# Kernel tuning notes

Measured on AMD Instinct MI355X. Metric: run time of the kernel, lower is better.

## Reference

```python
import jax, jax.numpy as jnp
from jax import lax
import numpy as np

B, C, L = 32, 8, 512
C_IN = 512      # must equal L (tokenConv consumes permuted tensor)
D_MODEL = 512
SCALE_NUM = 64  # 63 actual scales


def build_wavelet_bank(scale_num, LB=-8.0, UB=8.0, N=1024, Fb=2.0, Fc=8.0):
    """Replicates cmor_torch; returns centered zero-padded kernel bank [S, K].
    Zero-centering is exact because every kernel length (16*s+1) is odd and K is odd,
    so the padded conv with pad=(K-1)//2 equals the original per-scale conv with
    pad=(k-1)//2."""
    x = np.linspace(LB, UB, N)
    wav = (np.pi * Fb) ** (-0.5) * np.exp(2j * np.pi * Fc * x) * np.exp(-x ** 2 / Fb)
    step = x[1] - x[0]
    kernels = []
    for scale in np.arange(1, scale_num):
        j = (np.arange(scale * (x[-1] - x[0]) + 1) / (scale * step)).astype(int)
        j = j[j < wav.size]
        kernels.append(np.real(wav[j]) * scale ** (-0.5))
    K = max(len(k) for k in kernels)
    if K % 2 == 0:
        K += 1
    bank = np.zeros((len(kernels), K), np.float32)
    for i, k in enumerate(kernels):
        assert (K - len(k)) % 2 == 0, "kernel parity mismatch"
        off = (K - len(k)) // 2
        bank[i, off:off + len(k)] = k
    return bank


def setup_inputs() -> dict:
    key = jax.random.key(0)
    k1, k2 = jax.random.split(key)
    x = jax.random.normal(k1, (B, C, L), dtype=jnp.float32)
    wavelet_bank = jnp.asarray(build_wavelet_bank(SCALE_NUM))  # [63, K]
    token_w = jax.random.normal(k2, (D_MODEL, C_IN, 3), dtype=jnp.float32) * 0.02
    return {"x": x, "wavelet_bank": wavelet_bank, "token_w": token_w}


def reference(x, wavelet_bank, token_w):
    Bb, Cc, Ll = x.shape
    S, K = wavelet_bank.shape
    pad = (K - 1) // 2
    # fused CWT over all (channel, scale) pairs: [B*C, 1, L] conv [S, 1, K] -> [B*C, S, L]
    xr = x.reshape(Bb * Cc, 1, Ll)
    conv = lax.conv_general_dilated(
        xr, wavelet_bank[:, None, :], window_strides=(1,),
        padding=[(pad, pad)], dimension_numbers=("NCH", "OIH", "NCH"))
    d = jnp.abs(jnp.diff(conv, axis=-1))                 # [B*C, S, L-1]
    d = jnp.concatenate([d, d[..., -1:]], axis=-1)       # replicate last sample -> L
    feats = d.reshape(Bb, Cc * S, Ll)
    out = jnp.concatenate([x, feats], axis=1)            # [B, C*(1+S), L]
    # tokenConv on permuted tensor: channels = L (= c_in), length = C*(1+S)
    h = out.transpose(0, 2, 1)                           # [B, L, C_total]
    hp = jnp.concatenate([h[..., -1:], h, h[..., :1]], axis=-1)  # circular pad=1
    y = lax.conv_general_dilated(
        hp, token_w, window_strides=(1,), padding="VALID",
        dimension_numbers=("NCH", "OIH", "NCH"))         # [B, d_model, C_total]
    return y.transpose(0, 2, 1)                          # [B, C_total, d_model]
```

## Files before the change

kernel.cpp:

```cpp
#include <hip/hip_runtime.h>
#include <hip/hip_bf16.h>

#define NB 32
#define NC 8
#define NL 512
#define NS 63
#define NK 1009
#define NPAD 504
#define ND 512
#define NCT 512
#define NROWS 514

typedef __attribute__((ext_vector_type(4))) float f32x4;
typedef __attribute__((ext_vector_type(8))) short short8;
typedef __attribute__((ext_vector_type(4))) short short4v;

#define APAD_BYTES (NB * NROWS * NL * 2)
#define WB_BYTES   (3 * ND * NL * 2)
#define BANKB_BYTES (64 * 1024 * 2)

typedef const __attribute__((address_space(1))) unsigned int* gp1_t;
typedef __attribute__((address_space(3))) unsigned int* lp3_t;
__device__ __forceinline__ void gload_lds16(const void* g, void* l) {
  __builtin_amdgcn_global_load_lds((gp1_t)g, (lp3_t)l, 16, 0, 0);
}

__device__ __forceinline__ unsigned short bf16_bits(float v) {
  return __builtin_bit_cast(unsigned short, __float2bfloat16(v));
}

#define WAITVM(N) asm volatile("s_waitcnt vmcnt(" #N ")" ::: "memory")
#define FENCE() asm volatile("" ::: "memory")
#define BAR() __builtin_amdgcn_s_barrier()

__global__ __launch_bounds__(256) void prep_kernel(
    const float* __restrict__ bank, const float* __restrict__ tw,
    __hip_bfloat16* __restrict__ Wb, __hip_bfloat16* __restrict__ bankB) {
  const int idx = blockIdx.x * 256 + threadIdx.x;
  const int stride = gridDim.x * 256;

  for (int i = idx; i < ND * NL; i += stride) {
    float w0 = tw[i * 3 + 0];
    float w1 = tw[i * 3 + 1];
    float w2 = tw[i * 3 + 2];
    Wb[0 * ND * NL + i] = __float2bfloat16(w0);
    Wb[1 * ND * NL + i] = __float2bfloat16(w1);
    Wb[2 * ND * NL + i] = __float2bfloat16(w2);
  }
  for (int i = idx; i < 64 * 1024; i += stride) {
    int s = i >> 10;
    int k = i & 1023;
    float v = (s < NS && k < NK) ? bank[s * NK + k] : 0.f;
    bankB[i] = __float2bfloat16(v);
  }
}

#define CPY_STRIDE 3088

__global__ __launch_bounds__(512) void cwt_kernel(
    const float* __restrict__ x, const __hip_bfloat16* __restrict__ bankB,
    __hip_bfloat16* __restrict__ Apad) {
  __shared__ char smem[32768 + 4 * CPY_STRIDE];
  char* bankS = smem;
  char* cpy = smem + 32768;

  const int tid = threadIdx.x;
  const int bc = blockIdx.x;
  const int b = bc >> 3, c = bc & 7;
  const int w = tid >> 6, l = tid & 63;
  const int hi = l >> 4, li = l & 15;

  const float* xrow = x + bc * NL;

  {
    __hip_bfloat16 v = __float2bfloat16(xrow[tid & 511]);
    if (tid < 512) {
      Apad[((size_t)(b * NROWS) + 1 + c) * NL + tid] = v;
      if (c == 0) Apad[((size_t)(b * NROWS) + 513) * NL + tid] = v;
    }
  }

  for (int i = 0; i < 6; ++i) {
    int p = tid + i * 512;
    int r = p / 768, pe = p - r * 768;
    int e0 = 2 * pe;
    int i0 = e0 + r;
    float xa = (i0 >= NPAD && i0 < NPAD + NL) ? xrow[i0 - NPAD] : 0.f;
    float xb = (i0 + 1 >= NPAD && i0 + 1 < NPAD + NL) ? xrow[i0 + 1 - NPAD] : 0.f;
    float xc = (i0 + 2 >= NPAD && i0 + 2 < NPAD + NL) ? xrow[i0 + 2 - NPAD] : 0.f;
    unsigned short u0 = bf16_bits(xb - xa);
    unsigned short u1 = bf16_bits(xc - xb);
    *(unsigned int*)(cpy + r * CPY_STRIDE + e0 * 2) = (unsigned)u0 | ((unsigned)u1 << 16);
  }

#define STAGE(kt, buf)                                                        \
  {                                                                           \
    for (int i = 0; i < 2; ++i) {                                             \
      int ck = tid + i * 512;                                                 \
      int s_ = ck >> 4, rb = ck & 15;                                         \
      int srcc = rb ^ (s_ & 7);                                               \
      gload_lds16(bankB + s_ * 1024 + (kt) * 128 + srcc * 8,                  \
                  bankS + (buf) * 16384 + ck * 16);                           \
    }                                                                         \
  }

  STAGE(0, 0);
  __syncthreads();

  f32x4 acc[4][4] = {};
  const int r = l & 3;
  const int tbase = w * 64;
  int buf = 0;

  for (int kt = 0; kt < 8; ++kt) {
    if (kt < 7) STAGE(kt + 1, buf ^ 1);

#pragma unroll
    for (int ksl = 0; ksl < 4; ++ksl) {
      short8 av[4], bv[4];
#pragma unroll
      for (int m = 0; m < 4; ++m) {
        int srow = m * 16 + li;
        int chunk = (ksl * 4 + hi) ^ (srow & 7);
        av[m] = *(const short8*)(bankS + buf * 16384 + srow * 256 + chunk * 16);
      }
#pragma unroll
      for (int n = 0; n < 4; ++n) {
        int t = tbase + n * 16 + li;
        int e = t - r + kt * 128 + ksl * 32 + hi * 8;
        const char* pc = cpy + r * CPY_STRIDE + e * 2;
        short4v lo = *(const short4v*)pc;
        short4v hh = *(const short4v*)(pc + 8);
        short8 f;
        f[0] = lo[0]; f[1] = lo[1]; f[2] = lo[2]; f[3] = lo[3];
        f[4] = hh[0]; f[5] = hh[1]; f[6] = hh[2]; f[7] = hh[3];
        bv[n] = f;
      }
#pragma unroll
      for (int m = 0; m < 4; ++m)
#pragma unroll
        for (int n = 0; n < 4; ++n)
          acc[m][n] = __builtin_amdgcn_mfma_f32_16x16x32_bf16(av[m], bv[n], acc[m][n], 0, 0, 0);
    }

    if (kt < 7) {
      __syncthreads();
      buf ^= 1;
    }
  }

#pragma unroll
  for (int m = 0; m < 4; ++m) {
#pragma unroll
    for (int rg = 0; rg < 4; ++rg) {
      int s = m * 16 + hi * 4 + rg;
      if (s >= NS) continue;
      int ch = 8 + c * NS + s;
      size_t rowbase = ((size_t)(b * NROWS) + 1 + ch) * NL;
#pragma unroll
      for (int n = 0; n < 4; ++n) {
        int t = tbase + n * 16 + li;
        float d = fabsf(acc[m][n][rg]);
        __hip_bfloat16 hv = __float2bfloat16(d);
        bool lastgrp = (w == 7 && n == 3);
        bool skip = lastgrp && (li == 15);
        bool dup = lastgrp && (li == 14);
        if (!skip) Apad[rowbase + t] = hv;
        if (dup) Apad[rowbase + 511] = hv;
        if (ch == NCT - 1) {
          size_t wrapbase = (size_t)(b * NROWS) * NL;
          if (!skip) Apad[wrapbase + t] = hv;
          if (dup) Apad[wrapbase + 511] = hv;
        }
      }
    }
  }
#undef STAGE
}

__global__ __launch_bounds__(256) void gemm_kernel(
    const __hip_bfloat16* __restrict__ Ap, const __hip_bfloat16* __restrict__ Wb,
    float* __restrict__ out) {
  __shared__ __hip_bfloat16 sA[3][128 * 32];
  __shared__ __hip_bfloat16 sB[3][128 * 32];

  const int tid = threadIdx.x;
  const int b = blockIdx.y;
  const int tile = blockIdx.x;
  const int p0 = (tile & 3) * 128;
  const int o0 = (tile >> 2) * 128;

  const int w = tid >> 6, lane = tid & 63;
  const int wm = w >> 1, wn = w & 1;
  const int row_in = lane & 15, hi = lane >> 4;

  const int r0 = tid >> 2, cg0 = (tid & 3) ^ ((r0 >> 1) & 3);
  const int ck1 = tid + 256;
  const int r1 = ck1 >> 2, cg1 = (ck1 & 3) ^ ((r1 >> 1) & 3);

#define GSTAGE(kk, bu)                                                         \
  {                                                                            \
    const int kap_ = (kk) >> 4;                                                \
    const int l0_ = ((kk) & 15) << 5;                                          \
    gload_lds16(Ap + ((b * NROWS + p0 + kap_ + r0) * NL + l0_ + cg0 * 8),      \
                &sA[bu][tid * 8]);                                             \
    gload_lds16(Ap + ((b * NROWS + p0 + kap_ + r1) * NL + l0_ + cg1 * 8),      \
                &sA[bu][ck1 * 8]);                                             \
    gload_lds16(Wb + ((kap_ * ND + o0 + r0) * NL + l0_ + cg0 * 8),             \
                &sB[bu][tid * 8]);                                             \
    gload_lds16(Wb + ((kap_ * ND + o0 + r1) * NL + l0_ + cg1 * 8),             \
                &sB[bu][ck1 * 8]);                                             \
  }

#define COMPUTE(bu)                                                            \
  {                                                                            \
    short8 av[4], bv[4];                                                       \
    _Pragma("unroll") for (int m = 0; m < 4; ++m) {                            \
      int row = wm * 64 + m * 16 + row_in;                                     \
      int slot = row * 4 + (hi ^ ((row >> 1) & 3));                            \
      av[m] = *(const short8*)(&sA[bu][slot * 8]);                             \
    }                                                                          \
    _Pragma("unroll") for (int n = 0; n < 4; ++n) {                            \
      int row = wn * 64 + n * 16 + row_in;                                     \
      int slot = row * 4 + (hi ^ ((row >> 1) & 3));                            \
      bv[n] = *(const short8*)(&sB[bu][slot * 8]);                             \
    }                                                                          \
    _Pragma("unroll") for (int m = 0; m < 4; ++m)                              \
      _Pragma("unroll") for (int n = 0; n < 4; ++n)                            \
        acc[m][n] = __builtin_amdgcn_mfma_f32_16x16x32_bf16(av[m], bv[n],      \
                                                            acc[m][n], 0, 0, 0); \
  }

  f32x4 acc[4][4] = {};

  GSTAGE(0, 0);
  GSTAGE(1, 1);

  for (int g = 0; g < 15; ++g) {
    const int kk = g * 3;
    GSTAGE(kk + 2, 2); WAITVM(8); BAR(); FENCE(); COMPUTE(0); FENCE(); BAR();
    GSTAGE(kk + 3, 0); WAITVM(8); BAR(); FENCE(); COMPUTE(1); FENCE(); BAR();
    GSTAGE(kk + 4, 1); WAITVM(8); BAR(); FENCE(); COMPUTE(2); FENCE(); BAR();
  }
  GSTAGE(47, 2); WAITVM(8); BAR(); FENCE(); COMPUTE(0); FENCE(); BAR();
  WAITVM(4); BAR(); FENCE(); COMPUTE(1); FENCE(); BAR();
  WAITVM(0); BAR(); FENCE(); COMPUTE(2);
#undef GSTAGE
#undef COMPUTE

#pragma unroll
  for (int m = 0; m < 4; ++m) {
    const int p = p0 + wm * 64 + m * 16 + hi * 4;
#pragma unroll
    for (int n = 0; n < 4; ++n) {
      const int o = o0 + wn * 64 + n * 16 + row_in;
#pragma unroll
      for (int r = 0; r < 4; ++r)
        out[(size_t)((b * NCT) + p + r) * ND + o] = acc[m][n][r];
    }
  }
}

extern "C" void kernel_launch(void* const* d_in, const int* in_sizes, int n_in,
                              void* d_out, int out_size, void* d_ws, size_t ws_size,
                              hipStream_t stream) {
  const float* x = (const float*)d_in[0];
  const float* bank = (const float*)d_in[1];
  const float* tw = (const float*)d_in[2];
  float* out = (float*)d_out;

  char* ws = (char*)d_ws;
  __hip_bfloat16* Apad = (__hip_bfloat16*)ws;
  __hip_bfloat16* Wb = (__hip_bfloat16*)(ws + APAD_BYTES);
  __hip_bfloat16* bankB = (__hip_bfloat16*)(ws + APAD_BYTES + WB_BYTES);

  prep_kernel<<<512, 256, 0, stream>>>(bank, tw, Wb, bankB);
  cwt_kernel<<<256, 512, 0, stream>>>(x, bankB, Apad);
  gemm_kernel<<<dim3(16, 32), 256, 0, stream>>>(Apad, Wb, out);
}
```

Baseline: 68.57 us.

## Vectorize prep, preload whole CWT bank, 4-stage GEMM pipeline with block swizzle

The prep kernel now has each thread convert four weight triplets at once with float4 loads and ushort4 stores, and the launch shrinks to 256 blocks. The CWT kernel loads all eight bank K-tiles into 128KB of LDS up front and waits on them step by step with vmcnt, replacing the double-buffer loop and its syncs. The GEMM kernel moves to a 4-deep LDS ring with one barrier per stage and remaps block IDs so neighbouring blocks share batch tiles for better L2 reuse. The larger LDS footprints may reduce occupancy, and removing the trailing barrier relies on the 4-buffer distance to stay race-free.

```diff
diff --git a/kernel.cpp b/kernel.cpp
--- a/kernel.cpp
+++ b/kernel.cpp
@@ -37,21 +37,22 @@
     const float* __restrict__ bank, const float* __restrict__ tw,
     __hip_bfloat16* __restrict__ Wb, __hip_bfloat16* __restrict__ bankB) {
   const int idx = blockIdx.x * 256 + threadIdx.x;
-  const int stride = gridDim.x * 256;
-
-  for (int i = idx; i < ND * NL; i += stride) {
-    float w0 = tw[i * 3 + 0];
-    float w1 = tw[i * 3 + 1];
-    float w2 = tw[i * 3 + 2];
-    Wb[0 * ND * NL + i] = __float2bfloat16(w0);
-    Wb[1 * ND * NL + i] = __float2bfloat16(w1);
-    Wb[2 * ND * NL + i] = __float2bfloat16(w2);
-  }
-  for (int i = idx; i < 64 * 1024; i += stride) {
-    int s = i >> 10;
-    int k = i & 1023;
+
+  {
+    int i0 = idx * 4;
+    const float4* t4 = (const float4*)(tw + (size_t)i0 * 3);
+    float4 a = t4[0], bq = t4[1], c4 = t4[2];
+    ushort4 w0 = make_ushort4(bf16_bits(a.x), bf16_bits(a.w), bf16_bits(bq.z), bf16_bits(c4.y));
+    ushort4 w1 = make_ushort4(bf16_bits(a.y), bf16_bits(bq.x), bf16_bits(bq.w), bf16_bits(c4.z));
+    ushort4 w2 = make_ushort4(bf16_bits(a.z), bf16_bits(bq.y), bf16_bits(c4.x), bf16_bits(c4.w));
+    *(ushort4*)(Wb + 0 * ND * NL + i0) = w0;
+    *(ushort4*)(Wb + 1 * ND * NL + i0) = w1;
+    *(ushort4*)(Wb + 2 * ND * NL + i0) = w2;
+  }
+  {
+    int s = idx >> 10, k = idx & 1023;
     float v = (s < NS && k < NK) ? bank[s * NK + k] : 0.f;
-    bankB[i] = __float2bfloat16(v);
+    bankB[idx] = __float2bfloat16(v);
   }
 }
 
@@ -60,9 +61,9 @@
 __global__ __launch_bounds__(512) void cwt_kernel(
     const float* __restrict__ x, const __hip_bfloat16* __restrict__ bankB,
     __hip_bfloat16* __restrict__ Apad) {
-  __shared__ char smem[32768 + 4 * CPY_STRIDE];
+  __shared__ char smem[8 * 16384 + 4 * CPY_STRIDE];
   char* bankS = smem;
-  char* cpy = smem + 32768;
+  char* cpy = smem + 8 * 16384;
 
   const int tid = threadIdx.x;
   const int bc = blockIdx.x;
@@ -72,82 +73,79 @@
 
   const float* xrow = x + bc * NL;
 
-  {
-    __hip_bfloat16 v = __float2bfloat16(xrow[tid & 511]);
-    if (tid < 512) {
-      Apad[((size_t)(b * NROWS) + 1 + c) * NL + tid] = v;
-      if (c == 0) Apad[((size_t)(b * NROWS) + 513) * NL + tid] = v;
-    }
+  if (tid < 512) {
+    __hip_bfloat16 v = __float2bfloat16(xrow[tid]);
+    Apad[((size_t)(b * NROWS) + 1 + c) * NL + tid] = v;
+    if (c == 0) Apad[((size_t)(b * NROWS) + 513) * NL + tid] = v;
   }
 
   for (int i = 0; i < 6; ++i) {
     int p = tid + i * 512;
-    int r = p / 768, pe = p - r * 768;
+    int r_ = p / 768, pe = p - r_ * 768;
     int e0 = 2 * pe;
-    int i0 = e0 + r;
+    int i0 = e0 + r_;
     float xa = (i0 >= NPAD && i0 < NPAD + NL) ? xrow[i0 - NPAD] : 0.f;
     float xb = (i0 + 1 >= NPAD && i0 + 1 < NPAD + NL) ? xrow[i0 + 1 - NPAD] : 0.f;
     float xc = (i0 + 2 >= NPAD && i0 + 2 < NPAD + NL) ? xrow[i0 + 2 - NPAD] : 0.f;
     unsigned short u0 = bf16_bits(xb - xa);
     unsigned short u1 = bf16_bits(xc - xb);
-    *(unsigned int*)(cpy + r * CPY_STRIDE + e0 * 2) = (unsigned)u0 | ((unsigned)u1 << 16);
-  }
-
-#define STAGE(kt, buf)                                                        \
+    *(unsigned int*)(cpy + r_ * CPY_STRIDE + e0 * 2) = (unsigned)u0 | ((unsigned)u1 << 16);
+  }
+
+#define STAGE(kt)                                                             \
   {                                                                           \
     for (int i = 0; i < 2; ++i) {                                             \
       int ck = tid + i * 512;                                                 \
       int s_ = ck >> 4, rb = ck & 15;                                         \
       int srcc = rb ^ (s_ & 7);                                               \
       gload_lds16(bankB + s_ * 1024 + (kt) * 128 + srcc * 8,                  \
-                  bankS + (buf) * 16384 + ck * 16);                           \
+                  bankS + (kt) * 16384 + ck * 16);                            \
     }                                                                         \
   }
 
-  STAGE(0, 0);
-  __syncthreads();
+#define CCOMP(kt)                                                              \
+  {                                                                            \
+    _Pragma("unroll") for (int ksl = 0; ksl < 4; ++ksl) {                      \
+      short8 av[4], bv[4];                                                     \
+      _Pragma("unroll") for (int m = 0; m < 4; ++m) {                          \
+        int srow = m * 16 + li;                                                \
+        int chunk = (ksl * 4 + hi) ^ (srow & 7);                               \
+        av[m] = *(const short8*)(bankS + (kt) * 16384 + srow * 256 + chunk * 16); \
+      }                                                                        \
+      _Pragma("unroll") for (int n = 0; n < 4; ++n) {                          \
+        int t = tbase + n * 16 + li;                                           \
+        int e = t - r + (kt) * 128 + ksl * 32 + hi * 8;                        \
+        const char* pc = cpy + r * CPY_STRIDE + e * 2;                         \
+        short4v lo = *(const short4v*)pc;                                      \
+        short4v hh = *(const short4v*)(pc + 8);                                \
+        short8 f;                                                              \
+        f[0] = lo[0]; f[1] = lo[1]; f[2] = lo[2]; f[3] = lo[3];                \
+        f[4] = hh[0]; f[5] = hh[1]; f[6] = hh[2]; f[7] = hh[3];                \
+        bv[n] = f;                                                             \
+      }                                                                        \
+      _Pragma("unroll") for (int m = 0; m < 4; ++m)                            \
+        _Pragma("unroll") for (int n = 0; n < 4; ++n)                          \
+          acc[m][n] = __builtin_amdgcn_mfma_f32_16x16x32_bf16(av[m], bv[n],    \
+                                                              acc[m][n], 0, 0, 0); \
+    }                                                                          \
+  }
+
+  STAGE(0); STAGE(1); STAGE(2); STAGE(3);
+  STAGE(4); STAGE(5); STAGE(6); STAGE(7);
 
   f32x4 acc[4][4] = {};
   const int r = l & 3;
   const int tbase = w * 64;
-  int buf = 0;
-
-  for (int kt = 0; kt < 8; ++kt) {
-    if (kt < 7) STAGE(kt + 1, buf ^ 1);
-
-#pragma unroll
-    for (int ksl = 0; ksl < 4; ++ksl) {
-      short8 av[4], bv[4];
-#pragma unroll
-      for (int m = 0; m < 4; ++m) {
-        int srow = m * 16 + li;
-        int chunk = (ksl * 4 + hi) ^ (srow & 7);
-        av[m] = *(const short8*)(bankS + buf * 16384 + srow * 256 + chunk * 16);
-      }
-#pragma unroll
-      for (int n = 0; n < 4; ++n) {
-        int t = tbase + n * 16 + li;
-        int e = t - r + kt * 128 + ksl * 32 + hi * 8;
-        const char* pc = cpy + r * CPY_STRIDE + e * 2;
-        short4v lo = *(const short4v*)pc;
-        short4v hh = *(const short4v*)(pc + 8);
-        short8 f;
-        f[0] = lo[0]; f[1] = lo[1]; f[2] = lo[2]; f[3] = lo[3];
-        f[4] = hh[0]; f[5] = hh[1]; f[6] = hh[2]; f[7] = hh[3];
-        bv[n] = f;
-      }
-#pragma unroll
-      for (int m = 0; m < 4; ++m)
-#pragma unroll
-        for (int n = 0; n < 4; ++n)
-          acc[m][n] = __builtin_amdgcn_mfma_f32_16x16x32_bf16(av[m], bv[n], acc[m][n], 0, 0, 0);
-    }
-
-    if (kt < 7) {
-      __syncthreads();
-      buf ^= 1;
-    }
-  }
+
+  asm volatile("s_waitcnt vmcnt(14) lgkmcnt(0)" ::: "memory");
+  BAR(); FENCE(); CCOMP(0);
+  WAITVM(12); BAR(); FENCE(); CCOMP(1);
+  WAITVM(10); BAR(); FENCE(); CCOMP(2);
+  WAITVM(8);  BAR(); FENCE(); CCOMP(3);
+  WAITVM(6);  BAR(); FENCE(); CCOMP(4);
+  WAITVM(4);  BAR(); FENCE(); CCOMP(5);
+  WAITVM(2);  BAR(); FENCE(); CCOMP(6);
+  WAITVM(0);  BAR(); FENCE(); CCOMP(7);
 
 #pragma unroll
   for (int m = 0; m < 4; ++m) {
@@ -176,19 +174,22 @@
     }
   }
 #undef STAGE
+#undef CCOMP
 }
 
 __global__ __launch_bounds__(256) void gemm_kernel(
     const __hip_bfloat16* __restrict__ Ap, const __hip_bfloat16* __restrict__ Wb,
     float* __restrict__ out) {
-  __shared__ __hip_bfloat16 sA[3][128 * 32];
-  __shared__ __hip_bfloat16 sB[3][128 * 32];
+  __shared__ __hip_bfloat16 sA[4][128 * 32];
+  __shared__ __hip_bfloat16 sB[4][128 * 32];
 
   const int tid = threadIdx.x;
-  const int b = blockIdx.y;
-  const int tile = blockIdx.x;
-  const int p0 = (tile & 3) * 128;
-  const int o0 = (tile >> 2) * 128;
+  const int gid = blockIdx.x;
+  const int q = gid >> 3;
+  const int pid = (gid & 7) * 16 + (q >> 2);
+  const int b = pid >> 2;
+  const int p0 = (pid & 3) * 128;
+  const int o0 = (q & 3) * 128;
 
   const int w = tid >> 6, lane = tid & 63;
   const int wm = w >> 1, wn = w & 1;
@@ -236,15 +237,17 @@
   GSTAGE(0, 0);
   GSTAGE(1, 1);
 
-  for (int g = 0; g < 15; ++g) {
-    const int kk = g * 3;
-    GSTAGE(kk + 2, 2); WAITVM(8); BAR(); FENCE(); COMPUTE(0); FENCE(); BAR();
-    GSTAGE(kk + 3, 0); WAITVM(8); BAR(); FENCE(); COMPUTE(1); FENCE(); BAR();
-    GSTAGE(kk + 4, 1); WAITVM(8); BAR(); FENCE(); COMPUTE(2); FENCE(); BAR();
-  }
-  GSTAGE(47, 2); WAITVM(8); BAR(); FENCE(); COMPUTE(0); FENCE(); BAR();
-  WAITVM(4); BAR(); FENCE(); COMPUTE(1); FENCE(); BAR();
-  WAITVM(0); BAR(); FENCE(); COMPUTE(2);
+  for (int g = 0; g < 11; ++g) {
+    const int kk = g * 4;
+    GSTAGE(kk + 2, 2); WAITVM(8); BAR(); FENCE(); COMPUTE(0);
+    GSTAGE(kk + 3, 3); WAITVM(8); BAR(); FENCE(); COMPUTE(1);
+    GSTAGE(kk + 4, 0); WAITVM(8); BAR(); FENCE(); COMPUTE(2);
+    GSTAGE(kk + 5, 1); WAITVM(8); BAR(); FENCE(); COMPUTE(3);
+  }
+  GSTAGE(46, 2); WAITVM(8); BAR(); FENCE(); COMPUTE(0);
+  GSTAGE(47, 3); WAITVM(8); BAR(); FENCE(); COMPUTE(1);
+  WAITVM(4); BAR(); FENCE(); COMPUTE(2);
+  WAITVM(0); BAR(); FENCE(); COMPUTE(3);
 #undef GSTAGE
 #undef COMPUTE
 
@@ -274,7 +277,7 @@
   __hip_bfloat16* Wb = (__hip_bfloat16*)(ws + APAD_BYTES);
   __hip_bfloat16* bankB = (__hip_bfloat16*)(ws + APAD_BYTES + WB_BYTES);
 
-  prep_kernel<<<512, 256, 0, stream>>>(bank, tw, Wb, bankB);
+  prep_kernel<<<256, 256, 0, stream>>>(bank, tw, Wb, bankB);
   cwt_kernel<<<256, 512, 0, stream>>>(x, bankB, Apad);
-  gemm_kernel<<<dim3(16, 32), 256, 0, stream>>>(Apad, Wb, out);
-}
+  gemm_kernel<<<512, 256, 0, stream>>>(Apad, Wb, out);
+}
```

Measured after the change: 62.74 us. 8.5% less time.
